# Optimization experiments

Hardware: AMD Instinct MI355X
Metric: run time of the kernel (lower is better)

## Reference

```python
import jax, jax.numpy as jnp
import numpy as np

EMBED = 512
EXPAND = 1024


def setup_inputs() -> dict:
    key = jax.random.key(0)
    k1, k2, k3, k4, k5 = jax.random.split(key, 5)
    B, C, P, N = 4, EMBED, 16, 1024
    x = jax.random.normal(k1, (B, C, P, N), dtype=jnp.float32)
    # 1x1 conv weights == per-pixel linear maps over the channel dim
    Wqkv = jax.random.normal(k2, (1 + 2 * EXPAND, C), dtype=jnp.float32) * (1.0 / np.sqrt(C))
    bqkv = jax.random.normal(k3, (1 + 2 * EXPAND,), dtype=jnp.float32) * 0.01
    Wout = jax.random.normal(k4, (C, EXPAND), dtype=jnp.float32) * (1.0 / np.sqrt(EXPAND))
    bout = jax.random.normal(k5, (C,), dtype=jnp.float32) * 0.01
    return {"x": x, "Wqkv": Wqkv, "bqkv": bqkv, "Wout": Wout, "bout": bout}


def reference(x, Wqkv, bqkv, Wout, bout):
    # qkv 1x1 conv: (B,C,P,N) -> (B, 1+2E, P, N)
    qkv = jnp.einsum('oc,bcpn->bopn', Wqkv, x) + bqkv[None, :, None, None]
    E = EXPAND
    query = qkv[:, :1]            # (B,1,P,N)
    key_t = qkv[:, 1:1 + E]       # (B,E,P,N)
    value = qkv[:, 1 + E:]        # (B,E,P,N)
    # softmax over patches dim (last axis); attn_dropout p=0.0 -> identity
    context_scores = jax.nn.softmax(query, axis=-1)
    # weighted sum over N, keepdim -> (B,E,P,1)
    context_vector = jnp.sum(key_t * context_scores, axis=-1, keepdims=True)
    # broadcast gate
    out = jax.nn.relu(value) * context_vector  # (B,E,P,N)
    # out 1x1 conv back to embed channels
    out = jnp.einsum('oe,bepn->bopn', Wout, out) + bout[None, :, None, None]
    return out
```

## Files before the change

### kernel.cpp

```cpp
#include <hip/hip_runtime.h>

#define EMBED 512
#define EXPAND 1024
#define PNUM 16
#define NLEN 1024
#define CHW (PNUM * NLEN)
#define SLABS 64

typedef unsigned short u16;
typedef unsigned int u32;
typedef __bf16 bf16x8 __attribute__((ext_vector_type(8)));
typedef u16 u16x8 __attribute__((ext_vector_type(8)));
typedef float f32x4 __attribute__((ext_vector_type(4)));

__device__ __forceinline__ u16 f2bf(float f) {
  u32 u = __builtin_bit_cast(u32, f);
  return (u16)((u + 0x7FFFu + ((u >> 16) & 1u)) >> 16);
}
__device__ __forceinline__ float bf2f(u16 h) {
  return __builtin_bit_cast(float, (u32)h << 16);
}
__device__ __forceinline__ void gld16(const u16* g, u16* l) {
  __builtin_amdgcn_global_load_lds((__attribute__((address_space(1))) void*)g,
                                   (__attribute__((address_space(3))) void*)l,
                                   16, 0, 0);
}
__device__ __forceinline__ f32x4 MFMA(bf16x8 a, bf16x8 b, f32x4 c) {
  return __builtin_amdgcn_mfma_f32_16x16x32_bf16(a, b, c, 0, 0, 0);
}

__global__ __launch_bounds__(256) void k_convert_w(
    const float* __restrict__ Wqkv, const float* __restrict__ Wout,
    u16* __restrict__ WvB, u16* __restrict__ WoutB) {
  const int NV = EXPAND * EMBED;
  int idx = (blockIdx.x * 256 + threadIdx.x) * 4;
  if (idx < NV) {
    float4 v = *(const float4*)(Wqkv + (size_t)(1 + EXPAND) * EMBED + idx);
    uint2 u = make_uint2((u32)f2bf(v.x) | ((u32)f2bf(v.y) << 16),
                         (u32)f2bf(v.z) | ((u32)f2bf(v.w) << 16));
    *(uint2*)(WvB + idx) = u;
  } else {
    int j = idx - NV;
    float4 v = *(const float4*)(Wout + j);
    uint2 u = make_uint2((u32)f2bf(v.x) | ((u32)f2bf(v.y) << 16),
                         (u32)f2bf(v.z) | ((u32)f2bf(v.w) << 16));
    *(uint2*)(WoutB + j) = u;
  }
}

__global__ __launch_bounds__(256) void k_convert_x(
    const float* __restrict__ x, const float* __restrict__ Wqkv,
    float* __restrict__ q, u16* __restrict__ xbT) {
  __shared__ __align__(16) u16 tile[128 * 64];
  __shared__ float qp[256 * 4];
  const int slab = blockIdx.x >> 3, nw = blockIdx.x & 7;
  const int b = slab >> 4, p = slab & 15;
  const int t = threadIdx.x;
  const int c8 = t & 7;
  const int ng = t >> 3;
  const float* xs = x + (size_t)b * (EMBED * CHW) + (size_t)p * NLEN + nw * 128;
  u16* dst = xbT + (size_t)slab * (NLEN * EMBED) + (size_t)(nw * 128) * EMBED;
  float qa[4] = {0.f, 0.f, 0.f, 0.f};

  for (int cc = 0; cc < 8; ++cc) {
    const int cbase = cc * 64;
    float4 v[8];
#pragma unroll
    for (int k = 0; k < 8; ++k)
      v[k] = *(const float4*)(xs + (size_t)(cbase + c8 * 8 + k) * CHW + ng * 4);
    const float* w0 = Wqkv + cbase + c8 * 8;
#pragma unroll
    for (int k = 0; k < 8; ++k) {
      qa[0] += w0[k] * v[k].x;
      qa[1] += w0[k] * v[k].y;
      qa[2] += w0[k] * v[k].z;
      qa[3] += w0[k] * v[k].w;
    }
#pragma unroll
    for (int j = 0; j < 4; ++j) {
      const int nl = ng * 4 + j;
      float e[8];
#pragma unroll
      for (int k = 0; k < 8; ++k)
        e[k] = (j == 0) ? v[k].x : (j == 1) ? v[k].y : (j == 2) ? v[k].z : v[k].w;
      uint4 pk;
      pk.x = (u32)f2bf(e[0]) | ((u32)f2bf(e[1]) << 16);
      pk.y = (u32)f2bf(e[2]) | ((u32)f2bf(e[3]) << 16);
      pk.z = (u32)f2bf(e[4]) | ((u32)f2bf(e[5]) << 16);
      pk.w = (u32)f2bf(e[6]) | ((u32)f2bf(e[7]) << 16);
      *(uint4*)(tile + nl * 64 + ((c8 ^ (nl & 7)) << 3)) = pk;
    }
    __syncthreads();
#pragma unroll
    for (int m = 0; m < 4; ++m) {
      const int s = m * 256 + t;
      const int nl = s >> 3, ch = s & 7;
      uint4 vv = *(const uint4*)(tile + nl * 64 + ((ch ^ (nl & 7)) << 3));
      *(uint4*)(dst + (size_t)nl * EMBED + cbase + ch * 8) = vv;
    }
    __syncthreads();
  }
  qp[t * 4 + 0] = qa[0];
  qp[t * 4 + 1] = qa[1];
  qp[t * 4 + 2] = qa[2];
  qp[t * 4 + 3] = qa[3];
  __syncthreads();
  if (t < 128) {
    float a = 0.f;
#pragma unroll
    for (int o = 0; o < 8; ++o) a += qp[((((t >> 2) << 3) + o) << 2) + (t & 3)];
    q[(size_t)slab * NLEN + nw * 128 + t] = a;
  }
}

__global__ __launch_bounds__(256) void k_attn1(
    const float* __restrict__ q, const u16* __restrict__ xbT,
    float* __restrict__ ypart) {
  __shared__ float red[4];
  __shared__ float sm[256];
  __shared__ float yp[4][512];
  const int slab = blockIdx.x >> 2, qr = blockIdx.x & 3;
  const int t = threadIdx.x, w = t >> 6, l = t & 63;
  const float* qrow = q + (size_t)slab * NLEN;

  float4 q4 = ((const float4*)qrow)[t];
  float m = fmaxf(fmaxf(q4.x, q4.y), fmaxf(q4.z, q4.w));
#pragma unroll
  for (int sh = 32; sh; sh >>= 1) m = fmaxf(m, __shfl_xor(m, sh, 64));
  if (l == 0) red[w] = m;
  __syncthreads();
  float gm = fmaxf(fmaxf(red[0], red[1]), fmaxf(red[2], red[3]));
  float s = __expf(q4.x - gm) + __expf(q4.y - gm) + __expf(q4.z - gm) + __expf(q4.w - gm);
#pragma unroll
  for (int sh = 32; sh; sh >>= 1) s += __shfl_xor(s, sh, 64);
  __syncthreads();
  if (l == 0) red[w] = s;
  __syncthreads();
  float gs = red[0] + red[1] + red[2] + red[3];
  sm[t] = __expf(qrow[qr * 256 + t] - gm) / gs;
  __syncthreads();

  float ya[8] = {0.f, 0.f, 0.f, 0.f, 0.f, 0.f, 0.f, 0.f};
  const u16* xs = xbT + (size_t)slab * (NLEN * EMBED) + (size_t)qr * 256 * EMBED;
  for (int ni = 0; ni < 64; ++ni) {
    const int nloc = ni * 4 + w;
    const float sc = sm[nloc];
    u16x8 v = *(const u16x8*)(xs + (size_t)nloc * EMBED + l * 8);
#pragma unroll
    for (int j = 0; j < 8; ++j) ya[j] += sc * bf2f(v[j]);
  }
#pragma unroll
  for (int j = 0; j < 8; ++j) yp[w][l * 8 + j] = ya[j];
  __syncthreads();
  for (int c = t; c < 512; c += 256)
    ypart[((size_t)slab * 4 + qr) * 512 + c] = yp[0][c] + yp[1][c] + yp[2][c] + yp[3][c];
}

__global__ __launch_bounds__(256) void k_attn2(
    const float* __restrict__ ypart, const float* __restrict__ Wqkv,
    const float* __restrict__ bqkv, float* __restrict__ cv) {
  __shared__ float yl[512];
  const int slab = blockIdx.x >> 2, ec = blockIdx.x & 3;
  const int t = threadIdx.x;
  const int e = ec * 256 + t;
  const float* yb = ypart + (size_t)slab * 4 * 512;
  for (int c = t; c < 512; c += 256)
    yl[c] = yb[c] + yb[512 + c] + yb[1024 + c] + yb[1536 + c];
  __syncthreads();
  const float* wk = Wqkv + (size_t)(1 + e) * EMBED;
  float a = 0.f;
#pragma unroll 4
  for (int c0 = 0; c0 < EMBED; c0 += 4) {
    float4 wv = *(const float4*)(wk + c0);
    a += wv.x * yl[c0] + wv.y * yl[c0 + 1] + wv.z * yl[c0 + 2] + wv.w * yl[c0 + 3];
  }
  cv[(size_t)slab * EXPAND + e] = a + bqkv[1 + e];
}

template <int K, int NT>
__device__ __forceinline__ void gemm256(const u16* __restrict__ Abase,
                                        const u16* __restrict__ Bbase,
                                        u16* lds, f32x4 (&acc)[8][4]) {
  const int t = threadIdx.x;
  const int w = t >> 6, l = t & 63;
  const int wr = w >> 2, wc = w & 3;
  const int lr = l & 15, lj = l >> 4;
  const int rowA0 = wr * 128 + lr;
  const int rowB0 = wc * 64 + lr;

  auto stage2 = [&](u16* dstBase, const u16* gBase, int kt, int s0, int s1) {
    {
      const int s = s0 + t;
      const int row = s >> 3, pch = s & 7;
      gld16(gBase + (size_t)row * K + kt + ((pch ^ (row & 7)) << 3),
            dstBase + s * 8);
    }
    {
      const int s = s1 + t;
      const int row = s >> 3, pch = s & 7;
      gld16(gBase + (size_t)row * K + kt + ((pch ^ (row & 7)) << 3),
            dstBase + s * 8);
    }
  };
  auto rdA = [&](const u16* bufA, int mi, int kc) -> bf16x8 {
    const int row = rowA0 + mi * 16;
    const int ch = kc * 4 + lj;
    return *(const bf16x8*)(bufA + row * 64 + ((ch ^ (row & 7)) << 3));
  };
  auto rdB = [&](const u16* bufB, int ni, int kc) -> bf16x8 {
    const int row = rowB0 + ni * 16;
    const int ch = kc * 4 + lj;
    return *(const bf16x8*)(bufB + row * 64 + ((ch ^ (row & 7)) << 3));
  };

  u16* bA0 = lds;
  u16* bB0 = lds + 16384;
  u16* bA1 = lds + 32768;
  u16* bB1 = lds + 49152;

  stage2(bA0, Abase, 0, 0, 1024);
  stage2(bA0, Abase, 0, 512, 1536);
  stage2(bB0, Bbase, 0, 0, 512);
  stage2(bB0, Bbase, 0, 1024, 1536);
  stage2(bA1, Abase, 64, 0, 1024);
  stage2(bA1, Abase, 64, 512, 1536);
  stage2(bB1, Bbase, 64, 0, 512);
  stage2(bB1, Bbase, 64, 1024, 1536);
  asm volatile("s_waitcnt vmcnt(8)" ::: "memory");
  __builtin_amdgcn_s_barrier();

#pragma unroll 1
  for (int kt = 0; kt < NT; ++kt) {
    u16* bufA = lds + (kt & 1) * 32768;
    u16* bufB = bufA + 16384;
    const bool st2 = (kt + 2) < NT;
    const int k2 = (kt + 2) * 64;
    bf16x8 a0[4][2], a1[4][2], b0[2][2], b1[2][2];

#pragma unroll
    for (int mi = 0; mi < 4; ++mi)
#pragma unroll
      for (int kc = 0; kc < 2; ++kc) a0[mi][kc] = rdA(bufA, mi, kc);
#pragma unroll
    for (int ni = 0; ni < 2; ++ni)
#pragma unroll
      for (int kc = 0; kc < 2; ++kc) b0[ni][kc] = rdB(bufB, ni, kc);
    __builtin_amdgcn_s_barrier();
    __builtin_amdgcn_s_setprio(1);
#pragma unroll
    for (int mi = 0; mi < 4; ++mi)
#pragma unroll
      for (int ni = 0; ni < 2; ++ni)
#pragma unroll
        for (int kc = 0; kc < 2; ++kc)
          acc[mi][ni] = MFMA(a0[mi][kc], b0[ni][kc], acc[mi][ni]);
    __builtin_amdgcn_s_setprio(0);
    __builtin_amdgcn_s_barrier();

#pragma unroll
    for (int ni = 0; ni < 2; ++ni)
#pragma unroll
      for (int kc = 0; kc < 2; ++kc) b1[ni][kc] = rdB(bufB, ni + 2, kc);
    if (st2) {
      stage2(bufA, Abase, k2, 0, 1024);
      stage2(bufB, Bbase, k2, 0, 512);
    }
    __builtin_amdgcn_s_barrier();
    __builtin_amdgcn_s_setprio(1);
#pragma unroll
    for (int mi = 0; mi < 4; ++mi)
#pragma unroll
      for (int ni = 0; ni < 2; ++ni)
#pragma unroll
        for (int kc = 0; kc < 2; ++kc)
          acc[mi][ni + 2] = MFMA(a0[mi][kc], b1[ni][kc], acc[mi][ni + 2]);
    __builtin_amdgcn_s_setprio(0);
    __builtin_amdgcn_s_barrier();

#pragma unroll
    for (int mi = 0; mi < 4; ++mi)
#pragma unroll
      for (int kc = 0; kc < 2; ++kc) a1[mi][kc] = rdA(bufA, mi + 4, kc);
    if (st2) stage2(bufB, Bbase, k2, 1024, 1536);
    __builtin_amdgcn_s_barrier();
    __builtin_amdgcn_s_setprio(1);
#pragma unroll
    for (int mi = 0; mi < 4; ++mi)
#pragma unroll
      for (int ni = 0; ni < 2; ++ni)
#pragma unroll
        for (int kc = 0; kc < 2; ++kc)
          acc[mi + 4][ni + 2] = MFMA(a1[mi][kc], b1[ni][kc], acc[mi + 4][ni + 2]);
    __builtin_amdgcn_s_setprio(0);
    __builtin_amdgcn_s_barrier();

    if (st2) stage2(bufA, Abase, k2, 512, 1536);
    __builtin_amdgcn_s_barrier();
    __builtin_amdgcn_s_setprio(1);
#pragma unroll
    for (int mi = 0; mi < 4; ++mi)
#pragma unroll
      for (int ni = 0; ni < 2; ++ni)
#pragma unroll
        for (int kc = 0; kc < 2; ++kc)
          acc[mi + 4][ni] = MFMA(a1[mi][kc], b0[ni][kc], acc[mi + 4][ni]);
    __builtin_amdgcn_s_setprio(0);
    if (st2)
      asm volatile("s_waitcnt vmcnt(8)" ::: "memory");
    else
      asm volatile("s_waitcnt vmcnt(0)" ::: "memory");
    __builtin_amdgcn_s_barrier();
  }
}

__global__ __launch_bounds__(512, 2) void k_gemm1(
    const u16* __restrict__ xbT, const u16* __restrict__ WvB,
    const float* __restrict__ bqkv, const float* __restrict__ cv,
    u16* __restrict__ midT) {
  __shared__ __align__(16) u16 lds[65536];
  const int bid = blockIdx.x;
  const int xc = bid & 7, k = bid >> 3;
  const int te = k & 3;
  const int gg = ((k >> 2) << 3) | xc;
  const int slab = gg >> 2, tn = gg & 3;
  const u16* A = xbT + (size_t)slab * (NLEN * EMBED) + (size_t)tn * 256 * EMBED;
  const u16* B = WvB + (size_t)te * 256 * EMBED;
  f32x4 acc[8][4];
  const f32x4 z = {0.f, 0.f, 0.f, 0.f};
#pragma unroll
  for (int i = 0; i < 8; ++i)
#pragma unroll
    for (int j = 0; j < 4; ++j) acc[i][j] = z;
  gemm256<EMBED, 8>(A, B, lds, acc);

  const int t = threadIdx.x, w = t >> 6, l = t & 63;
  const int wr = w >> 2, wc = w & 3;
  const int lr = l & 15, lq4 = (l >> 4) * 4;
#pragma unroll
  for (int ni = 0; ni < 4; ++ni) {
    const int col = wc * 64 + ni * 16 + lr;
    const int e = te * 256 + col;
    const float bv = bqkv[1 + EXPAND + e];
    const float cve = cv[(size_t)slab * EXPAND + e];
#pragma unroll
    for (int mi = 0; mi < 8; ++mi) {
      const int nr = wr * 128 + mi * 16 + lq4;
#pragma unroll
      for (int r = 0; r < 4; ++r) {
        float v = acc[mi][ni][r] + bv;
        v = v > 0.f ? v * cve : 0.f;
        const int row = nr + r;
        lds[row * 256 + ((((col >> 3) ^ (row & 7)) << 3) | (col & 7))] = f2bf(v);
      }
    }
  }
  __syncthreads();
  u16* mt = midT + (size_t)slab * (NLEN * EXPAND) + (size_t)te * 256;
#pragma unroll
  for (int it = 0; it < 16; ++it) {
    const int row = w * 32 + it * 2 + (l >> 5);
    const int ch = (l & 31) ^ (row & 7);
    uint4 v = *(const uint4*)(lds + row * 256 + ch * 8);
    *(uint4*)(mt + (size_t)(tn * 256 + row) * EXPAND + (l & 31) * 8) = v;
  }
}

__global__ __launch_bounds__(512, 2) void k_gemm2(
    const u16* __restrict__ midT, const u16* __restrict__ WoutB,
    const float* __restrict__ bout, float* __restrict__ out) {
  __shared__ __align__(16) u16 lds[65536];
  const int bid = blockIdx.x;
  const int xc = bid & 7, k = bid >> 3;
  const int to = k & 1;
  const int gg = ((k >> 1) << 3) | xc;
  const int slab = gg >> 2, tn = gg & 3;
  const int b = slab >> 4, p = slab & 15;
  const u16* A = midT + (size_t)slab * (NLEN * EXPAND) + (size_t)tn * 256 * EXPAND;
  const u16* B = WoutB + (size_t)to * 256 * EXPAND;
  f32x4 acc[8][4];
  const f32x4 z = {0.f, 0.f, 0.f, 0.f};
#pragma unroll
  for (int i = 0; i < 8; ++i)
#pragma unroll
    for (int j = 0; j < 4; ++j) acc[i][j] = z;
  gemm256<EXPAND, 16>(A, B, lds, acc);

  const int t = threadIdx.x, w = t >> 6, l = t & 63;
  const int wr = w >> 2, wc = w & 3;
  const int lr = l & 15, lq4 = (l >> 4) * 4;
  float* ob = out + (size_t)b * (EMBED * CHW) + (size_t)p * NLEN;
#pragma unroll
  for (int ni = 0; ni < 4; ++ni) {
    const int o = to * 256 + wc * 64 + ni * 16 + lr;
    const float bo = bout[o];
#pragma unroll
    for (int mi = 0; mi < 8; ++mi) {
      const int nr = tn * 256 + wr * 128 + mi * 16 + lq4;
      float4 v;
      v.x = acc[mi][ni][0] + bo;
      v.y = acc[mi][ni][1] + bo;
      v.z = acc[mi][ni][2] + bo;
      v.w = acc[mi][ni][3] + bo;
      *(float4*)(ob + (size_t)o * CHW + nr) = v;
    }
  }
}

extern "C" void kernel_launch(void* const* d_in, const int* in_sizes, int n_in,
                              void* d_out, int out_size, void* d_ws, size_t ws_size,
                              hipStream_t stream) {
  const float* x = (const float*)d_in[0];
  const float* Wqkv = (const float*)d_in[1];
  const float* bqkv = (const float*)d_in[2];
  const float* Wout = (const float*)d_in[3];
  const float* bout = (const float*)d_in[4];
  float* out = (float*)d_out;

  char* ws = (char*)d_ws;
  u16* xbT = (u16*)ws;
  u16* WvB = (u16*)(ws + 67108864);
  u16* WoutB = (u16*)(ws + 68157440);
  float* q = (float*)(ws + 69206016);
  float* cv = (float*)(ws + 69468160);
  u16* midT = (u16*)(ws + 69730304);
  float* ypart = (float*)(ws + 69730304);

  k_convert_w<<<1024, 256, 0, stream>>>(Wqkv, Wout, WvB, WoutB);
  k_convert_x<<<512, 256, 0, stream>>>(x, Wqkv, q, xbT);
  k_attn1<<<256, 256, 0, stream>>>(q, xbT, ypart);
  k_attn2<<<256, 256, 0, stream>>>(ypart, Wqkv, bqkv, cv);
  k_gemm1<<<1024, 512, 0, stream>>>(xbT, WvB, bqkv, cv, midT);
  k_gemm2<<<512, 512, 0, stream>>>(midT, WoutB, bout, out);
}
```

Before: 270.8 us.

## Split convert_x and attn1 over more blocks; precompute GEMM LDS offsets

k_convert_x now splits the channel dimension in half across twice as many blocks, writing partial query sums that k_attn1 adds together. k_attn1 splits the N range into 8 chunks instead of 4, doubling its grid, and k_attn2 sums 8 partials instead of 4. The GEMM helper precomputes its swizzled LDS read offsets and global-load offsets once into registers rather than recomputing them every iteration. The extra blocks are meant to fill the GPU in the memory-bound front stages, at the cost of more partial-sum traffic and higher register pressure in the GEMM.

```diff
diff --git a/kernel.cpp b/kernel.cpp
--- a/kernel.cpp
+++ b/kernel.cpp
@@ -50,10 +50,12 @@
 
 __global__ __launch_bounds__(256) void k_convert_x(
     const float* __restrict__ x, const float* __restrict__ Wqkv,
-    float* __restrict__ q, u16* __restrict__ xbT) {
+    float* __restrict__ qpart, u16* __restrict__ xbT) {
   __shared__ __align__(16) u16 tile[128 * 64];
   __shared__ float qp[256 * 4];
-  const int slab = blockIdx.x >> 3, nw = blockIdx.x & 7;
+  const int slab = blockIdx.x >> 4;
+  const int nw = (blockIdx.x >> 1) & 7;
+  const int chalf = blockIdx.x & 1;
   const int b = slab >> 4, p = slab & 15;
   const int t = threadIdx.x;
   const int c8 = t & 7;
@@ -62,8 +64,8 @@
   u16* dst = xbT + (size_t)slab * (NLEN * EMBED) + (size_t)(nw * 128) * EMBED;
   float qa[4] = {0.f, 0.f, 0.f, 0.f};
 
-  for (int cc = 0; cc < 8; ++cc) {
-    const int cbase = cc * 64;
+  for (int cc = 0; cc < 4; ++cc) {
+    const int cbase = chalf * 256 + cc * 64;
     float4 v[8];
 #pragma unroll
     for (int k = 0; k < 8; ++k)
@@ -109,21 +111,24 @@
     float a = 0.f;
 #pragma unroll
     for (int o = 0; o < 8; ++o) a += qp[((((t >> 2) << 3) + o) << 2) + (t & 3)];
-    q[(size_t)slab * NLEN + nw * 128 + t] = a;
+    qpart[(size_t)slab * 2048 + chalf * 1024 + nw * 128 + t] = a;
   }
 }
 
 __global__ __launch_bounds__(256) void k_attn1(
-    const float* __restrict__ q, const u16* __restrict__ xbT,
+    const float* __restrict__ qpart, const u16* __restrict__ xbT,
     float* __restrict__ ypart) {
   __shared__ float red[4];
-  __shared__ float sm[256];
+  __shared__ float sm[128];
   __shared__ float yp[4][512];
-  const int slab = blockIdx.x >> 2, qr = blockIdx.x & 3;
+  const int slab = blockIdx.x >> 3, n8 = blockIdx.x & 7;
   const int t = threadIdx.x, w = t >> 6, l = t & 63;
-  const float* qrow = q + (size_t)slab * NLEN;
-
-  float4 q4 = ((const float4*)qrow)[t];
+  const float* q0 = qpart + (size_t)slab * 2048;
+  const float* q1 = q0 + 1024;
+
+  float4 qa = ((const float4*)q0)[t];
+  float4 qb = ((const float4*)q1)[t];
+  float4 q4 = make_float4(qa.x + qb.x, qa.y + qb.y, qa.z + qb.z, qa.w + qb.w);
   float m = fmaxf(fmaxf(q4.x, q4.y), fmaxf(q4.z, q4.w));
 #pragma unroll
   for (int sh = 32; sh; sh >>= 1) m = fmaxf(m, __shfl_xor(m, sh, 64));
@@ -137,12 +142,15 @@
   if (l == 0) red[w] = s;
   __syncthreads();
   float gs = red[0] + red[1] + red[2] + red[3];
-  sm[t] = __expf(qrow[qr * 256 + t] - gm) / gs;
+  if (t < 128) {
+    const int n = n8 * 128 + t;
+    sm[t] = __expf(q0[n] + q1[n] - gm) / gs;
+  }
   __syncthreads();
 
   float ya[8] = {0.f, 0.f, 0.f, 0.f, 0.f, 0.f, 0.f, 0.f};
-  const u16* xs = xbT + (size_t)slab * (NLEN * EMBED) + (size_t)qr * 256 * EMBED;
-  for (int ni = 0; ni < 64; ++ni) {
+  const u16* xs = xbT + (size_t)slab * (NLEN * EMBED) + (size_t)(n8 * 128) * EMBED;
+  for (int ni = 0; ni < 32; ++ni) {
     const int nloc = ni * 4 + w;
     const float sc = sm[nloc];
     u16x8 v = *(const u16x8*)(xs + (size_t)nloc * EMBED + l * 8);
@@ -153,7 +161,7 @@
   for (int j = 0; j < 8; ++j) yp[w][l * 8 + j] = ya[j];
   __syncthreads();
   for (int c = t; c < 512; c += 256)
-    ypart[((size_t)slab * 4 + qr) * 512 + c] = yp[0][c] + yp[1][c] + yp[2][c] + yp[3][c];
+    ypart[((size_t)slab * 8 + n8) * 512 + c] = yp[0][c] + yp[1][c] + yp[2][c] + yp[3][c];
 }
 
 __global__ __launch_bounds__(256) void k_attn2(
@@ -163,9 +171,13 @@
   const int slab = blockIdx.x >> 2, ec = blockIdx.x & 3;
   const int t = threadIdx.x;
   const int e = ec * 256 + t;
-  const float* yb = ypart + (size_t)slab * 4 * 512;
-  for (int c = t; c < 512; c += 256)
-    yl[c] = yb[c] + yb[512 + c] + yb[1024 + c] + yb[1536 + c];
+  const float* yb = ypart + (size_t)slab * 8 * 512;
+  for (int c = t; c < 512; c += 256) {
+    float a = 0.f;
+#pragma unroll
+    for (int k = 0; k < 8; ++k) a += yb[k * 512 + c];
+    yl[c] = a;
+  }
   __syncthreads();
   const float* wk = Wqkv + (size_t)(1 + e) * EMBED;
   float a = 0.f;
@@ -185,32 +197,32 @@
   const int w = t >> 6, l = t & 63;
   const int wr = w >> 2, wc = w & 3;
   const int lr = l & 15, lj = l >> 4;
-  const int rowA0 = wr * 128 + lr;
-  const int rowB0 = wc * 64 + lr;
-
-  auto stage2 = [&](u16* dstBase, const u16* gBase, int kt, int s0, int s1) {
-    {
-      const int s = s0 + t;
-      const int row = s >> 3, pch = s & 7;
-      gld16(gBase + (size_t)row * K + kt + ((pch ^ (row & 7)) << 3),
-            dstBase + s * 8);
-    }
-    {
-      const int s = s1 + t;
-      const int row = s >> 3, pch = s & 7;
-      gld16(gBase + (size_t)row * K + kt + ((pch ^ (row & 7)) << 3),
-            dstBase + s * 8);
-    }
-  };
-  auto rdA = [&](const u16* bufA, int mi, int kc) -> bf16x8 {
-    const int row = rowA0 + mi * 16;
-    const int ch = kc * 4 + lj;
-    return *(const bf16x8*)(bufA + row * 64 + ((ch ^ (row & 7)) << 3));
-  };
-  auto rdB = [&](const u16* bufB, int ni, int kc) -> bf16x8 {
-    const int row = rowB0 + ni * 16;
-    const int ch = kc * 4 + lj;
-    return *(const bf16x8*)(bufB + row * 64 + ((ch ^ (row & 7)) << 3));
+
+  int oa[8][2], ob[4][2];
+#pragma unroll
+  for (int mi = 0; mi < 8; ++mi)
+#pragma unroll
+    for (int kc = 0; kc < 2; ++kc) {
+      const int row = wr * 128 + mi * 16 + lr;
+      oa[mi][kc] = row * 64 + (((kc * 4 + lj) ^ (row & 7)) << 3);
+    }
+#pragma unroll
+  for (int ni = 0; ni < 4; ++ni)
+#pragma unroll
+    for (int kc = 0; kc < 2; ++kc) {
+      const int row = wc * 64 + ni * 16 + lr;
+      ob[ni][kc] = row * 64 + (((kc * 4 + lj) ^ (row & 7)) << 3);
+    }
+  int gofs[4], dofs[4];
+#pragma unroll
+  for (int i = 0; i < 4; ++i) {
+    const int s = i * 512 + t;
+    const int row = s >> 3, pch = s & 7;
+    gofs[i] = row * K + ((pch ^ (row & 7)) << 3);
+    dofs[i] = s * 8;
+  }
+  auto st1 = [&](u16* dstBase, const u16* gBase, int kt, int i) {
+    gld16(gBase + gofs[i] + kt, dstBase + dofs[i]);
   };
 
   u16* bA0 = lds;
@@ -218,14 +230,14 @@
   u16* bA1 = lds + 32768;
   u16* bB1 = lds + 49152;
 
-  stage2(bA0, Abase, 0, 0, 1024);
-  stage2(bA0, Abase, 0, 512, 1536);
-  stage2(bB0, Bbase, 0, 0, 512);
-  stage2(bB0, Bbase, 0, 1024, 1536);
-  stage2(bA1, Abase, 64, 0, 1024);
-  stage2(bA1, Abase, 64, 512, 1536);
-  stage2(bB1, Bbase, 64, 0, 512);
-  stage2(bB1, Bbase, 64, 1024, 1536);
+  st1(bA0, Abase, 0, 0); st1(bA0, Abase, 0, 1);
+  st1(bA0, Abase, 0, 2); st1(bA0, Abase, 0, 3);
+  st1(bB0, Bbase, 0, 0); st1(bB0, Bbase, 0, 1);
+  st1(bB0, Bbase, 0, 2); st1(bB0, Bbase, 0, 3);
+  st1(bA1, Abase, 64, 0); st1(bA1, Abase, 64, 1);
+  st1(bA1, Abase, 64, 2); st1(bA1, Abase, 64, 3);
+  st1(bB1, Bbase, 64, 0); st1(bB1, Bbase, 64, 1);
+  st1(bB1, Bbase, 64, 2); st1(bB1, Bbase, 64, 3);
   asm volatile("s_waitcnt vmcnt(8)" ::: "memory");
   __builtin_amdgcn_s_barrier();
 
@@ -240,11 +252,13 @@
 #pragma unroll
     for (int mi = 0; mi < 4; ++mi)
 #pragma unroll
-      for (int kc = 0; kc < 2; ++kc) a0[mi][kc] = rdA(bufA, mi, kc);
+      for (int kc = 0; kc < 2; ++kc)
+        a0[mi][kc] = *(const bf16x8*)(bufA + oa[mi][kc]);
 #pragma unroll
     for (int ni = 0; ni < 2; ++ni)
 #pragma unroll
-      for (int kc = 0; kc < 2; ++kc) b0[ni][kc] = rdB(bufB, ni, kc);
+      for (int kc = 0; kc < 2; ++kc)
+        b0[ni][kc] = *(const bf16x8*)(bufB + ob[ni][kc]);
     __builtin_amdgcn_s_barrier();
     __builtin_amdgcn_s_setprio(1);
 #pragma unroll
@@ -260,10 +274,11 @@
 #pragma unroll
     for (int ni = 0; ni < 2; ++ni)
 #pragma unroll
-      for (int kc = 0; kc < 2; ++kc) b1[ni][kc] = rdB(bufB, ni + 2, kc);
+      for (int kc = 0; kc < 2; ++kc)
+        b1[ni][kc] = *(const bf16x8*)(bufB + ob[ni + 2][kc]);
     if (st2) {
-      stage2(bufA, Abase, k2, 0, 1024);
-      stage2(bufB, Bbase, k2, 0, 512);
+      st1(bufA, Abase, k2, 0); st1(bufA, Abase, k2, 2);
+      st1(bufB, Bbase, k2, 0); st1(bufB, Bbase, k2, 1);
     }
     __builtin_amdgcn_s_barrier();
     __builtin_amdgcn_s_setprio(1);
@@ -280,8 +295,9 @@
 #pragma unroll
     for (int mi = 0; mi < 4; ++mi)
 #pragma unroll
-      for (int kc = 0; kc < 2; ++kc) a1[mi][kc] = rdA(bufA, mi + 4, kc);
-    if (st2) stage2(bufB, Bbase, k2, 1024, 1536);
+      for (int kc = 0; kc < 2; ++kc)
+        a1[mi][kc] = *(const bf16x8*)(bufA + oa[mi + 4][kc]);
+    if (st2) { st1(bufB, Bbase, k2, 2); st1(bufB, Bbase, k2, 3); }
     __builtin_amdgcn_s_barrier();
     __builtin_amdgcn_s_setprio(1);
 #pragma unroll
@@ -294,7 +310,7 @@
     __builtin_amdgcn_s_setprio(0);
     __builtin_amdgcn_s_barrier();
 
-    if (st2) stage2(bufA, Abase, k2, 512, 1536);
+    if (st2) { st1(bufA, Abase, k2, 1); st1(bufA, Abase, k2, 3); }
     __builtin_amdgcn_s_barrier();
     __builtin_amdgcn_s_setprio(1);
 #pragma unroll
@@ -420,14 +436,14 @@
   u16* xbT = (u16*)ws;
   u16* WvB = (u16*)(ws + 67108864);
   u16* WoutB = (u16*)(ws + 68157440);
-  float* q = (float*)(ws + 69206016);
   float* cv = (float*)(ws + 69468160);
   u16* midT = (u16*)(ws + 69730304);
   float* ypart = (float*)(ws + 69730304);
+  float* qpart = (float*)(ws + 69730304 + 1048576);
 
   k_convert_w<<<1024, 256, 0, stream>>>(Wqkv, Wout, WvB, WoutB);
-  k_convert_x<<<512, 256, 0, stream>>>(x, Wqkv, q, xbT);
-  k_attn1<<<256, 256, 0, stream>>>(q, xbT, ypart);
+  k_convert_x<<<1024, 256, 0, stream>>>(x, Wqkv, qpart, xbT);
+  k_attn1<<<512, 256, 0, stream>>>(qpart, xbT, ypart);
   k_attn2<<<256, 256, 0, stream>>>(ypart, Wqkv, bqkv, cv);
   k_gemm1<<<1024, 512, 0, stream>>>(xbT, WvB, bqkv, cv, midT);
   k_gemm2<<<512, 512, 0, stream>>>(midT, WoutB, bout, out);
```

After: 272.3 us. About the same (+0.6%).
